# Kernel optimization log

Hardware: AMD Instinct MI355X
Metric: run time of the kernel (lower is better)

The kernel has to match this reference:

```python
import jax, jax.numpy as jnp
import numpy as np
import math

N_HEAD = 8
N_FEAT = 512
D_K = N_FEAT // N_HEAD
B, T = 4, 2048


def setup_inputs() -> dict:
    key = jax.random.key(0)
    ks = jax.random.split(key, 16)
    s = 1.0 / math.sqrt(N_FEAT)
    return {
        "x": jax.random.normal(ks[0], (B, T, N_FEAT), dtype=jnp.float32),
        "pos_emb": jax.random.normal(ks[1], (1, T, N_FEAT), dtype=jnp.float32),
        "Wq": jax.random.normal(ks[2], (N_FEAT, N_FEAT), dtype=jnp.float32) * s,
        "bq": jnp.zeros((N_FEAT,), dtype=jnp.float32),
        "Wk": jax.random.normal(ks[3], (N_FEAT, N_FEAT), dtype=jnp.float32) * s,
        "bk": jnp.zeros((N_FEAT,), dtype=jnp.float32),
        "Wv": jax.random.normal(ks[4], (N_FEAT, N_FEAT), dtype=jnp.float32) * s,
        "bv": jnp.zeros((N_FEAT,), dtype=jnp.float32),
        "Wpos": jax.random.normal(ks[5], (N_FEAT, N_FEAT), dtype=jnp.float32) * s,
        "Wout": jax.random.normal(ks[6], (N_FEAT, N_FEAT), dtype=jnp.float32) * s,
        "bout": jnp.zeros((N_FEAT,), dtype=jnp.float32),
        "pos_bias_u": jax.random.normal(ks[7], (N_HEAD, D_K), dtype=jnp.float32) * 0.05,
        "pos_bias_v": jax.random.normal(ks[8], (N_HEAD, D_K), dtype=jnp.float32) * 0.05,
    }


def reference(x, pos_emb, Wq, bq, Wk, bk, Wv, bv, Wpos, Wout, bout,
              pos_bias_u, pos_bias_v):
    b, t, f = x.shape
    h, d = N_HEAD, D_K
    # QKV projections (torch Linear: y = x @ W.T + b), split into heads -> (B,H,T,d)
    q = (jnp.einsum('btf,of->bto', x, Wq) + bq).reshape(b, t, h, d).transpose(0, 2, 1, 3)
    k = (jnp.einsum('btf,of->bto', x, Wk) + bk).reshape(b, t, h, d).transpose(0, 2, 1, 3)
    v = (jnp.einsum('btf,of->bto', x, Wv) + bv).reshape(b, t, h, d).transpose(0, 2, 1, 3)
    # positional projection: (1, T_pos, F) -> (H, T_pos, d)
    tp = pos_emb.shape[1]
    p = jnp.einsum('ptf,of->pto', pos_emb, Wpos).reshape(tp, h, d).transpose(1, 0, 2)
    q_u = q + pos_bias_u[None, :, None, :]  # (B,H,T,d)
    q_v = q + pos_bias_v[None, :, None, :]
    matrix_ac = jnp.einsum('bhtd,bhsd->bhts', q_u, k)   # content-content
    matrix_bd = jnp.einsum('bhtd,hsd->bhts', q_v, p)    # content-position
    scores = (matrix_ac + matrix_bd) / math.sqrt(d)
    attn = jax.nn.softmax(scores, axis=-1)  # dropout is identity in eval mode
    out = jnp.einsum('bhts,bhsd->bhtd', attn, v)
    out = out.transpose(0, 2, 1, 3).reshape(b, t, h * d)
    return jnp.einsum('btf,of->bto', out, Wout) + bout
```

## Files before the change

kernel.cpp:

```cpp
#include <hip/hip_runtime.h>

typedef float f4 __attribute__((ext_vector_type(4)));
typedef __attribute__((ext_vector_type(8))) short bf16x8;
typedef __attribute__((ext_vector_type(4))) float f32x4;
typedef __attribute__((ext_vector_type(2))) int i32x2;

#define T_SEQ 2048
#define NFEAT 512
#define NHEAD 8
#define DK    64
#define BATCH 4

using gptr_t = const __attribute__((address_space(1))) void*;
using lptr_t = __attribute__((address_space(3))) void*;

#define LOG2E_8 0.18033688011f

static __device__ __forceinline__ short f2bf(float f) {
    unsigned u = __builtin_bit_cast(unsigned, f);
    u += 0x7fff + ((u >> 16) & 1);
    return (short)(u >> 16);
}
static __device__ __forceinline__ float b2f(short s) {
    unsigned u = ((unsigned)(unsigned short)s) << 16;
    return __builtin_bit_cast(float, u);
}
static __device__ __forceinline__ int pkbf(float a, float b) {
    unsigned ua = __builtin_bit_cast(unsigned, a) + 0x8000u;
    unsigned ub = __builtin_bit_cast(unsigned, b) + 0x8000u;
    return (int)((ua >> 16) | (ub & 0xFFFF0000u));
}

__global__ __launch_bounds__(256) void cvt_kernel(
    const float* __restrict__ x, const float* __restrict__ pos,
    const float* __restrict__ Wq, const float* __restrict__ Wk, const float* __restrict__ Wv,
    const float* __restrict__ Wpos, const float* __restrict__ Wout,
    const float* __restrict__ bq, const float* __restrict__ bk, const float* __restrict__ bv,
    short* __restrict__ xb, short* __restrict__ posb, short* __restrict__ wqkv,
    short* __restrict__ wpb, short* __restrict__ wob, float* __restrict__ bqkv)
{
    const int blk = blockIdx.x;
    const float* src; short* dst; int off;
    if      (blk < 2048) { src = x;    dst = xb;          off = blk * 2048; }
    else if (blk < 2560) { src = pos;  dst = posb;        off = (blk - 2048) * 2048; }
    else if (blk < 2688) { src = Wq;   dst = wqkv;        off = (blk - 2560) * 2048; }
    else if (blk < 2816) { src = Wk;   dst = wqkv + 262144; off = (blk - 2688) * 2048; }
    else if (blk < 2944) { src = Wv;   dst = wqkv + 524288; off = (blk - 2816) * 2048; }
    else if (blk < 3072) { src = Wpos; dst = wpb;         off = (blk - 2944) * 2048; }
    else if (blk < 3200) { src = Wout; dst = wob;         off = (blk - 3072) * 2048; }
    else {
        int t = threadIdx.x;
        bqkv[t]        = bq[t];        bqkv[256 + t]  = bq[256 + t];
        bqkv[512 + t]  = bk[t];        bqkv[768 + t]  = bk[256 + t];
        bqkv[1024 + t] = bv[t];        bqkv[1280 + t] = bv[256 + t];
        return;
    }
    int i = off + threadIdx.x * 8;
    f4 a = *(const f4*)(src + i);
    f4 b = *(const f4*)(src + i + 4);
    bf16x8 o;
#pragma unroll
    for (int j = 0; j < 4; ++j) { o[j] = f2bf(a[j]); o[4 + j] = f2bf(b[j]); }
    *(bf16x8*)(dst + i) = o;
}

template<int OUT_BF16>
static __device__ __forceinline__ void gemm_tile(
    short* As, short* Bs,
    const short* __restrict__ A, const short* __restrict__ B,
    const float* __restrict__ bias, void* __restrict__ Cv,
    int N, int K, int row0, int col0)
{
    const int tid = threadIdx.x, lane = tid & 63, wave = tid >> 6;
    const int col = lane & 15, quad = lane >> 4;
    const int wm = (wave >> 1) * 64, wn = (wave & 1) * 64;
    const int rl = lane & 15;

    const short* Abase = A + (size_t)(row0 + wave * 32 + rl) * K + (lane >> 4) * 8;
    const short* Bbase = B + (size_t)(col0 + wave * 32 + rl) * K + (lane >> 4) * 8;

    f32x4 acc[4][4];
#pragma unroll
    for (int i = 0; i < 4; ++i)
#pragma unroll
        for (int j = 0; j < 4; ++j) acc[i][j] = (f32x4){0.f, 0.f, 0.f, 0.f};

    for (int k0 = 0; k0 < K; k0 += 64) {
        __syncthreads();
#pragma unroll
        for (int c = 0; c < 2; ++c)
#pragma unroll
            for (int hf = 0; hf < 2; ++hf) {
                __builtin_amdgcn_global_load_lds((gptr_t)(Abase + (size_t)(16 * c) * K + k0 + hf * 32),
                                                 (lptr_t)(As + wave * 2048 + c * 1024 + hf * 512), 16, 0, 0);
                __builtin_amdgcn_global_load_lds((gptr_t)(Bbase + (size_t)(16 * c) * K + k0 + hf * 32),
                                                 (lptr_t)(Bs + wave * 2048 + c * 1024 + hf * 512), 16, 0, 0);
            }
        __syncthreads();
#pragma unroll
        for (int kt = 0; kt < 2; ++kt) {
            bf16x8 af[4], bfr[4];
#pragma unroll
            for (int mt = 0; mt < 4; ++mt)
                af[mt] = *(const bf16x8*)&As[((wm >> 4) + mt) * 1024 + (kt * 4 + quad) * 128 + col * 8];
#pragma unroll
            for (int nt = 0; nt < 4; ++nt)
                bfr[nt] = *(const bf16x8*)&Bs[((wn >> 4) + nt) * 1024 + (kt * 4 + quad) * 128 + col * 8];
#pragma unroll
            for (int mt = 0; mt < 4; ++mt)
#pragma unroll
                for (int nt = 0; nt < 4; ++nt)
                    acc[mt][nt] = __builtin_amdgcn_mfma_f32_16x16x32_bf16(af[mt], bfr[nt], acc[mt][nt], 0, 0, 0);
        }
    }

    float bv4[4];
#pragma unroll
    for (int nt = 0; nt < 4; ++nt)
        bv4[nt] = bias ? bias[col0 + wn + nt * 16 + col] : 0.f;
#pragma unroll
    for (int mt = 0; mt < 4; ++mt)
#pragma unroll
        for (int reg = 0; reg < 4; ++reg) {
            int r = row0 + wm + mt * 16 + quad * 4 + reg;
#pragma unroll
            for (int nt = 0; nt < 4; ++nt) {
                int c = col0 + wn + nt * 16 + col;
                float v = acc[mt][nt][reg] + bv4[nt];
                if (OUT_BF16) ((short*)Cv)[(size_t)r * N + c] = f2bf(v);
                else          ((float*)Cv)[(size_t)r * N + c] = v;
            }
        }
}

__global__ __launch_bounds__(256) void gemm_qkv_pos(
    const short* __restrict__ xb, const short* __restrict__ wqkv,
    const float* __restrict__ bqkv, short* __restrict__ QKV,
    const short* __restrict__ posb, const short* __restrict__ wpb,
    short* __restrict__ Pm)
{
    __shared__ short As[8192], Bs[8192];
    const int bid = blockIdx.x;
    if (bid < 768) {
        const int xcd = bid & 7, s = bid >> 3;
        const int row = xcd * 8 + (s & 7), colt = s >> 3;
        gemm_tile<1>(As, Bs, xb, wqkv, bqkv, QKV, 1536, 512, row * 128, colt * 128);
    } else {
        const int t = bid - 768;
        gemm_tile<1>(As, Bs, posb, wpb, nullptr, Pm, 512, 512, (t / 4) * 128, (t % 4) * 128);
    }
}

__global__ __launch_bounds__(256) void gemm_out_kernel(
    const short* __restrict__ A, const short* __restrict__ B,
    const float* __restrict__ bias, float* __restrict__ C)
{
    __shared__ short As[8192], Bs[8192];
    const int bid = blockIdx.x;
    const int xcd = bid & 7, s = bid >> 3;
    const int row = xcd * 8 + (s & 7), colt = s >> 3;
    gemm_tile<0>(As, Bs, A, B, bias, C, 512, 512, row * 128, colt * 128);
}

__global__ __launch_bounds__(256) void kvprep_kernel(
    const short* __restrict__ qkv, const short* __restrict__ pm,
    const float* __restrict__ u, const float* __restrict__ vb,
    short* __restrict__ kp, short* __restrict__ vt, float* __restrict__ cb)
{
    __shared__ short tile[64][72];
    const int tid = threadIdx.x, lr = tid >> 2, lc = (tid & 3) * 16;
    const int bh = blockIdx.y, b = bh >> 3, h = bh & 7, s0 = blockIdx.x * 64;

    const short* kptr = qkv + (size_t)(b * T_SEQ + s0 + lr) * 1536 + 512 + h * DK + lc;
    const short* pptr = pm + (size_t)(s0 + lr) * NFEAT + h * DK + lc;
    const short* vptr = qkv + (size_t)(b * T_SEQ + s0 + lr) * 1536 + 1024 + h * DK + lc;
    bf16x8 k0_ = *(const bf16x8*)kptr,       k1_ = *(const bf16x8*)(kptr + 8);
    bf16x8 p0_ = *(const bf16x8*)pptr,       p1_ = *(const bf16x8*)(pptr + 8);
    bf16x8 v0_ = *(const bf16x8*)vptr,       v1_ = *(const bf16x8*)(vptr + 8);

    float c = 0.f;
    bf16x8 o0, o1;
#pragma unroll
    for (int j = 0; j < 8; ++j) {
        float kf = b2f(k0_[j]), pf = b2f(p0_[j]);
        o0[j] = f2bf(kf + pf);
        c += u[h * DK + lc + j] * kf + vb[h * DK + lc + j] * pf;
        float kf1 = b2f(k1_[j]), pf1 = b2f(p1_[j]);
        o1[j] = f2bf(kf1 + pf1);
        c += u[h * DK + lc + 8 + j] * kf1 + vb[h * DK + lc + 8 + j] * pf1;
    }
    short* kpd = kp + ((size_t)bh * T_SEQ + s0 + lr) * DK + lc;
    *(bf16x8*)kpd       = o0;
    *(bf16x8*)(kpd + 8) = o1;
    c += __shfl_xor(c, 1);
    c += __shfl_xor(c, 2);
    if ((tid & 3) == 0) cb[(size_t)bh * T_SEQ + s0 + lr] = LOG2E_8 * c;

    *(bf16x8*)&tile[lr][lc]     = v0_;
    *(bf16x8*)&tile[lr][lc + 8] = v1_;
    __syncthreads();
    short* dst = vt + (size_t)(bh * DK + lr) * T_SEQ + s0 + lc;
    bf16x8 t0_, t1_;
#pragma unroll
    for (int j = 0; j < 8; ++j) { t0_[j] = tile[lc + j][lr]; t1_[j] = tile[lc + 8 + j][lr]; }
    *(bf16x8*)dst       = t0_;
    *(bf16x8*)(dst + 8) = t1_;
}

__global__ __launch_bounds__(256, 4) void attn_kernel(
    const short* __restrict__ qkv, const short* __restrict__ kp,
    const short* __restrict__ vt, const float* __restrict__ cb,
    short* __restrict__ Op, float* __restrict__ Lb)
{
    __shared__ __align__(16) short KPs[64][72], Vts[64][72], Ps[4][32][72];
    __shared__ float cs[64];
    const int tid = threadIdx.x, lane = tid & 63, wave = tid >> 6;
    const int col = lane & 15, quad = lane >> 4;
    const int idx = blockIdx.x;
    const int xcd = idx & 7, slot = idx >> 3;
    const int half = slot & 1;
    const int t0 = ((slot >> 1) & 15) * 128;
    const int bh = (slot >> 5) * 8 + xcd;
    const int base = half * 1024;
    const int b = bh >> 3, h = bh & 7;

    bf16x8 qa[2][2];
#pragma unroll
    for (int g = 0; g < 2; ++g) {
        const short* qb = qkv + (size_t)(b * T_SEQ + t0 + wave * 32 + g * 16 + col) * 1536 + h * DK + quad * 8;
        qa[g][0] = *(const bf16x8*)qb;
        qa[g][1] = *(const bf16x8*)(qb + 32);
    }

    const int lr  = tid >> 2;
    const int lcq = (tid & 3) * 16;
    const int rho = 4 * (lr & 15) + (lr >> 4);

    const short* kpbase = kp + (size_t)bh * T_SEQ * DK;
    const short* vtbase = vt + (size_t)bh * DK * T_SEQ;

    bf16x8 kpr0 = *(const bf16x8*)(kpbase + (size_t)(base + rho) * DK + lcq);
    bf16x8 kpr1 = *(const bf16x8*)(kpbase + (size_t)(base + rho) * DK + lcq + 8);
    bf16x8 vtr0 = *(const bf16x8*)(vtbase + (size_t)lr * T_SEQ + base + lcq);
    bf16x8 vtr1 = *(const bf16x8*)(vtbase + (size_t)lr * T_SEQ + base + lcq + 8);
    float cbr = (tid < 64) ? cb[(size_t)bh * T_SEQ + base + tid] : 0.f;

    f32x4 Oacc[2][4];
    float lsum[2][4];
#pragma unroll
    for (int g = 0; g < 2; ++g)
#pragma unroll
        for (int i = 0; i < 4; ++i) { Oacc[g][i] = (f32x4){0.f, 0.f, 0.f, 0.f}; lsum[g][i] = 0.f; }

    for (int it = 0; it < 16; ++it) {
        __syncthreads();
        *(bf16x8*)&KPs[lr][lcq]     = kpr0;
        *(bf16x8*)&KPs[lr][lcq + 8] = kpr1;
        *(bf16x8*)&Vts[lr][lcq]     = vtr0;
        *(bf16x8*)&Vts[lr][lcq + 8] = vtr1;
        if (tid < 64) cs[tid] = cbr;
        __syncthreads();

        const int sn = base + (((it + 1) & 15) << 6);
        kpr0 = *(const bf16x8*)(kpbase + (size_t)(sn + rho) * DK + lcq);
        kpr1 = *(const bf16x8*)(kpbase + (size_t)(sn + rho) * DK + lcq + 8);
        vtr0 = *(const bf16x8*)(vtbase + (size_t)lr * T_SEQ + sn + lcq);
        vtr1 = *(const bf16x8*)(vtbase + (size_t)lr * T_SEQ + sn + lcq + 8);
        if (tid < 64) cbr = cb[(size_t)bh * T_SEQ + sn + tid];

        f32x4 S[2][4];
#pragma unroll
        for (int g = 0; g < 2; ++g)
#pragma unroll
            for (int nt = 0; nt < 4; ++nt) S[g][nt] = (f32x4){0.f, 0.f, 0.f, 0.f};
#pragma unroll
        for (int nt = 0; nt < 4; ++nt) {
            bf16x8 b0 = *(const bf16x8*)&KPs[nt * 16 + col][quad * 8];
            bf16x8 b1 = *(const bf16x8*)&KPs[nt * 16 + col][32 + quad * 8];
            S[0][nt] = __builtin_amdgcn_mfma_f32_16x16x32_bf16(qa[0][0], b0, S[0][nt], 0, 0, 0);
            S[1][nt] = __builtin_amdgcn_mfma_f32_16x16x32_bf16(qa[1][0], b0, S[1][nt], 0, 0, 0);
            S[0][nt] = __builtin_amdgcn_mfma_f32_16x16x32_bf16(qa[0][1], b1, S[0][nt], 0, 0, 0);
            S[1][nt] = __builtin_amdgcn_mfma_f32_16x16x32_bf16(qa[1][1], b1, S[1][nt], 0, 0, 0);
        }
        const f4 cv = *(const f4*)&cs[4 * col];
#pragma unroll
        for (int g = 0; g < 2; ++g)
#pragma unroll
            for (int reg = 0; reg < 4; ++reg) {
                float e0 = __builtin_amdgcn_exp2f(fmaf(S[g][0][reg], LOG2E_8, cv[0]));
                float e1 = __builtin_amdgcn_exp2f(fmaf(S[g][1][reg], LOG2E_8, cv[1]));
                float e2 = __builtin_amdgcn_exp2f(fmaf(S[g][2][reg], LOG2E_8, cv[2]));
                float e3 = __builtin_amdgcn_exp2f(fmaf(S[g][3][reg], LOG2E_8, cv[3]));
                lsum[g][reg] += (e0 + e1) + (e2 + e3);
                i32x2 pw; pw[0] = pkbf(e0, e1); pw[1] = pkbf(e2, e3);
                *(i32x2*)&Ps[wave][g * 16 + quad * 4 + reg][4 * col] = pw;
            }
#pragma unroll
        for (int kt = 0; kt < 2; ++kt) {
            bf16x8 pa0 = *(const bf16x8*)&Ps[wave][col][kt * 32 + quad * 8];
            bf16x8 pa1 = *(const bf16x8*)&Ps[wave][16 + col][kt * 32 + quad * 8];
#pragma unroll
            for (int dt = 0; dt < 4; ++dt) {
                bf16x8 vb = *(const bf16x8*)&Vts[dt * 16 + col][kt * 32 + quad * 8];
                Oacc[0][dt] = __builtin_amdgcn_mfma_f32_16x16x32_bf16(pa0, vb, Oacc[0][dt], 0, 0, 0);
                Oacc[1][dt] = __builtin_amdgcn_mfma_f32_16x16x32_bf16(pa1, vb, Oacc[1][dt], 0, 0, 0);
            }
        }
    }
    short* ophalf = Op + (size_t)half * 4194304;
    float* lhalf  = Lb + (size_t)half * 65536 + (size_t)bh * T_SEQ;
#pragma unroll
    for (int g = 0; g < 2; ++g)
#pragma unroll
        for (int reg = 0; reg < 4; ++reg) {
            float l = lsum[g][reg];
#pragma unroll
            for (int off = 1; off < 16; off <<= 1) l += __shfl_xor(l, off);
            int t = t0 + wave * 32 + g * 16 + quad * 4 + reg;
            if (col == 0) lhalf[t] = l;
            short* op = ophalf + (size_t)(b * T_SEQ + t) * NFEAT + h * DK;
#pragma unroll
            for (int dt = 0; dt < 4; ++dt)
                op[dt * 16 + col] = f2bf(Oacc[g][dt][reg]);
        }
}

__global__ __launch_bounds__(256) void combine_kernel(
    const short* __restrict__ Op, const float* __restrict__ Lb,
    short* __restrict__ attO)
{
    const int e = blockIdx.x * 256 + threadIdx.x;
    const int flat = e * 8;
    const int r = flat >> 9, c = flat & 511;
    const int bh = ((r >> 11) << 3) + (c >> 6);
    const int t = r & 2047;
    const float l = Lb[bh * T_SEQ + t] + Lb[65536 + bh * T_SEQ + t];
    const float inv = 1.f / l;
    bf16x8 o1 = *(const bf16x8*)(Op + flat);
    bf16x8 o2 = *(const bf16x8*)(Op + 4194304 + flat);
    bf16x8 o;
#pragma unroll
    for (int j = 0; j < 8; ++j) o[j] = f2bf((b2f(o1[j]) + b2f(o2[j])) * inv);
    *(bf16x8*)(attO + flat) = o;
}

extern "C" void kernel_launch(void* const* d_in, const int* in_sizes, int n_in,
                              void* d_out, int out_size, void* d_ws, size_t ws_size,
                              hipStream_t stream)
{
    const float* x    = (const float*)d_in[0];
    const float* pos  = (const float*)d_in[1];
    const float* Wq   = (const float*)d_in[2];
    const float* bq   = (const float*)d_in[3];
    const float* Wk   = (const float*)d_in[4];
    const float* bk   = (const float*)d_in[5];
    const float* Wv   = (const float*)d_in[6];
    const float* bv   = (const float*)d_in[7];
    const float* Wpos = (const float*)d_in[8];
    const float* Wout = (const float*)d_in[9];
    const float* bout = (const float*)d_in[10];
    const float* pbu  = (const float*)d_in[11];
    const float* pbv  = (const float*)d_in[12];
    float* out = (float*)d_out;

    short* xb   = (short*)d_ws;
    short* posb = xb   + 4194304;
    short* wqkv = posb + 1048576;
    short* wpb  = wqkv + 786432;
    short* wob  = wpb  + 262144;
    short* QKV  = wob  + 262144;
    short* Pm   = QKV  + 12582912;
    short* KP   = Pm   + 1048576;
    short* Vt   = KP   + 4194304;
    short* AttO = Vt   + 4194304;
    float* bqkv = (float*)(AttO + 4194304);
    float* Cb   = bqkv + 1536;
    short* Op   = (short*)(Cb + 65536);
    float* Lb   = (float*)(Op + 8388608);

    cvt_kernel<<<dim3(3201), dim3(256), 0, stream>>>(x, pos, Wq, Wk, Wv, Wpos, Wout, bq, bk, bv,
                                                     xb, posb, wqkv, wpb, wob, bqkv);
    gemm_qkv_pos<<<dim3(832), dim3(256), 0, stream>>>(xb, wqkv, bqkv, QKV, posb, wpb, Pm);
    kvprep_kernel<<<dim3(T_SEQ / 64, BATCH * NHEAD), dim3(256), 0, stream>>>(QKV, Pm, pbu, pbv, KP, Vt, Cb);
    attn_kernel<<<dim3(1024), dim3(256), 0, stream>>>(QKV, KP, Vt, Cb, Op, Lb);
    combine_kernel<<<dim3(2048), dim3(256), 0, stream>>>(Op, Lb, AttO);
    gemm_out_kernel<<<dim3(256), dim3(256), 0, stream>>>(AttO, wob, bout, out);
}
```

Measured before the change: 214.0 us.

## Fuse split-KV combine into output projection GEMM with smaller tiles

Removes the separate combine kernel and the AttO intermediate buffer. The output-projection GEMM now reads both partial attention outputs and their softmax denominators directly, sums and normalizes them while staging the A tile into LDS, then multiplies by Wout. The tile drops from 128x128 to 64x64 with 1024 blocks and a simple register-prefetch loop. This saves a launch and a full round trip of the attention output through memory, at the cost of a simpler, less tuned GEMM inner loop and repeated normalization work across column tiles.

Measured after the change: 221.3 us. 3.4% more time.

```diff
diff --git a/kernel.cpp b/kernel.cpp
--- a/kernel.cpp
+++ b/kernel.cpp
@@ -151,17 +151,6 @@
     }
 }
 
-__global__ __launch_bounds__(256) void gemm_out_kernel(
-    const short* __restrict__ A, const short* __restrict__ B,
-    const float* __restrict__ bias, float* __restrict__ C)
-{
-    __shared__ short As[8192], Bs[8192];
-    const int bid = blockIdx.x;
-    const int xcd = bid & 7, s = bid >> 3;
-    const int row = xcd * 8 + (s & 7), colt = s >> 3;
-    gemm_tile<0>(As, Bs, A, B, bias, C, 512, 512, row * 128, colt * 128);
-}
-
 __global__ __launch_bounds__(256) void kvprep_kernel(
     const short* __restrict__ qkv, const short* __restrict__ pm,
     const float* __restrict__ u, const float* __restrict__ vb,
@@ -325,23 +314,78 @@
         }
 }
 
-__global__ __launch_bounds__(256) void combine_kernel(
+__global__ __launch_bounds__(256) void gemm_out_fused(
     const short* __restrict__ Op, const float* __restrict__ Lb,
-    short* __restrict__ attO)
-{
-    const int e = blockIdx.x * 256 + threadIdx.x;
-    const int flat = e * 8;
-    const int r = flat >> 9, c = flat & 511;
-    const int bh = ((r >> 11) << 3) + (c >> 6);
-    const int t = r & 2047;
-    const float l = Lb[bh * T_SEQ + t] + Lb[65536 + bh * T_SEQ + t];
-    const float inv = 1.f / l;
-    bf16x8 o1 = *(const bf16x8*)(Op + flat);
-    bf16x8 o2 = *(const bf16x8*)(Op + 4194304 + flat);
-    bf16x8 o;
-#pragma unroll
-    for (int j = 0; j < 8; ++j) o[j] = f2bf((b2f(o1[j]) + b2f(o2[j])) * inv);
-    *(bf16x8*)(attO + flat) = o;
+    const short* __restrict__ B, const float* __restrict__ bias,
+    float* __restrict__ C)
+{
+    __shared__ __align__(16) short As[4096], Bs[4096];
+    const int tid = threadIdx.x, lane = tid & 63, wave = tid >> 6;
+    const int col = lane & 15, quad = lane >> 4;
+    const int rl = lane & 15, kc = lane >> 4;
+    const int bid = blockIdx.x;
+    const int xcd = bid & 7, s = bid >> 3;
+    const int row0 = (xcd * 16 + (s & 15)) * 64;
+    const int col0 = (s >> 4) * 64;
+
+    const int r  = row0 + wave * 16 + rl;
+    const int bb = r >> 11, tt = r & 2047;
+    const short* Abase  = Op +           (size_t)r * 512 + kc * 8;
+    const short* A2base = Op + 4194304 + (size_t)r * 512 + kc * 8;
+    const short* Bbase  = B + (size_t)(col0 + wave * 16 + rl) * 512 + kc * 8;
+    const float* L1 = Lb + bb * 16384 + tt;
+    const float* L2 = Lb + 65536 + bb * 16384 + tt;
+
+    f32x4 acc[4];
+#pragma unroll
+    for (int j = 0; j < 4; ++j) acc[j] = (f32x4){0.f, 0.f, 0.f, 0.f};
+
+    bf16x8 a1[2], a2[2], bg[2];
+    a1[0] = *(const bf16x8*)(Abase);   a1[1] = *(const bf16x8*)(Abase + 32);
+    a2[0] = *(const bf16x8*)(A2base);  a2[1] = *(const bf16x8*)(A2base + 32);
+    bg[0] = *(const bf16x8*)(Bbase);   bg[1] = *(const bf16x8*)(Bbase + 32);
+    float l1 = L1[0], l2 = L2[0];
+
+    for (int k0 = 0; k0 < 512; k0 += 64) {
+        const float inv = 1.f / (l1 + l2);
+        bf16x8 pa[2];
+#pragma unroll
+        for (int hf = 0; hf < 2; ++hf)
+#pragma unroll
+            for (int j = 0; j < 8; ++j)
+                pa[hf][j] = f2bf((b2f(a1[hf][j]) + b2f(a2[hf][j])) * inv);
+        __syncthreads();
+        *(bf16x8*)&As[wave * 1024 + kc * 128 + rl * 8]       = pa[0];
+        *(bf16x8*)&As[wave * 1024 + 512 + kc * 128 + rl * 8] = pa[1];
+        *(bf16x8*)&Bs[wave * 1024 + kc * 128 + rl * 8]       = bg[0];
+        *(bf16x8*)&Bs[wave * 1024 + 512 + kc * 128 + rl * 8] = bg[1];
+        __syncthreads();
+        const int kn = (k0 + 64) & 511;
+        a1[0] = *(const bf16x8*)(Abase + kn);   a1[1] = *(const bf16x8*)(Abase + kn + 32);
+        a2[0] = *(const bf16x8*)(A2base + kn);  a2[1] = *(const bf16x8*)(A2base + kn + 32);
+        bg[0] = *(const bf16x8*)(Bbase + kn);   bg[1] = *(const bf16x8*)(Bbase + kn + 32);
+        const int hk = kn >> 6;
+        l1 = L1[hk * 2048]; l2 = L2[hk * 2048];
+#pragma unroll
+        for (int kt = 0; kt < 2; ++kt) {
+            bf16x8 af = *(const bf16x8*)&As[wave * 1024 + (kt * 4 + quad) * 128 + col * 8];
+#pragma unroll
+            for (int nt = 0; nt < 4; ++nt) {
+                bf16x8 bfr = *(const bf16x8*)&Bs[nt * 1024 + (kt * 4 + quad) * 128 + col * 8];
+                acc[nt] = __builtin_amdgcn_mfma_f32_16x16x32_bf16(af, bfr, acc[nt], 0, 0, 0);
+            }
+        }
+    }
+    float bv4[4];
+#pragma unroll
+    for (int nt = 0; nt < 4; ++nt) bv4[nt] = bias[col0 + nt * 16 + col];
+#pragma unroll
+    for (int reg = 0; reg < 4; ++reg) {
+        int rr = row0 + wave * 16 + quad * 4 + reg;
+#pragma unroll
+        for (int nt = 0; nt < 4; ++nt)
+            C[(size_t)rr * 512 + col0 + nt * 16 + col] = acc[nt][reg] + bv4[nt];
+    }
 }
 
 extern "C" void kernel_launch(void* const* d_in, const int* in_sizes, int n_in,
@@ -372,8 +416,7 @@
     short* Pm   = QKV  + 12582912;
     short* KP   = Pm   + 1048576;
     short* Vt   = KP   + 4194304;
-    short* AttO = Vt   + 4194304;
-    float* bqkv = (float*)(AttO + 4194304);
+    float* bqkv = (float*)(Vt + 4194304);
     float* Cb   = bqkv + 1536;
     short* Op   = (short*)(Cb + 65536);
     float* Lb   = (float*)(Op + 8388608);
@@ -383,6 +426,5 @@
     gemm_qkv_pos<<<dim3(832), dim3(256), 0, stream>>>(xb, wqkv, bqkv, QKV, posb, wpb, Pm);
     kvprep_kernel<<<dim3(T_SEQ / 64, BATCH * NHEAD), dim3(256), 0, stream>>>(QKV, Pm, pbu, pbv, KP, Vt, Cb);
     attn_kernel<<<dim3(1024), dim3(256), 0, stream>>>(QKV, KP, Vt, Cb, Op, Lb);
-    combine_kernel<<<dim3(2048), dim3(256), 0, stream>>>(Op, Lb, AttO);
-    gemm_out_kernel<<<dim3(256), dim3(256), 0, stream>>>(AttO, wob, bout, out);
-}
+    gemm_out_fused<<<dim3(1024), dim3(256), 0, stream>>>(Op, Lb, wob, bout, out);
+}
```
